# Performance work log

Hardware: AMD Instinct MI355X
Metric: run time of the kernel (lower is better)

## Reference

```python
import jax, jax.numpy as jnp
import numpy as np


def setup_inputs() -> dict:
    key = jax.random.key(0)
    k0, k1, k2, k3, k4 = jax.random.split(key, 5)
    B, d_inner, L, d_state = 64, 384, 197, 16
    x = jax.random.normal(k0, (B, d_inner, L), dtype=jnp.float32)
    # deltaA = exp(delta*A) lies in (0,1); uniform keeps the recurrence stable
    deltaA = jax.random.uniform(k1, (B, d_inner, L, d_state), dtype=jnp.float32)
    deltaB = jax.random.normal(k2, (B, d_inner, L, d_state), dtype=jnp.float32)
    C = jax.random.normal(k3, (B, d_state, L), dtype=jnp.float32)
    D = jax.random.normal(k4, (d_inner,), dtype=jnp.float32)
    return {"x": x, "deltaA": deltaA, "deltaB": deltaB, "C": C, "D": D}


def reference(x, deltaA, deltaB, C, D):
    """Selective scan: h_t = deltaB_t*x_t + deltaA_t*h_{t-1}; y_t = h_t @ C_t.
    x:(B,d,L) deltaA/deltaB:(B,d,L,n) C:(B,n,L) D:(d,)
    """
    deltaB_x = deltaB * x[..., None]              # (B,d,L,n)
    dA_t = jnp.moveaxis(deltaA, 2, 0)             # (L,B,d,n)
    dBx_t = jnp.moveaxis(deltaB_x, 2, 0)          # (L,B,d,n)
    C_t = jnp.moveaxis(C, 2, 0)                   # (L,B,n)

    def step(h, inputs):
        a, bx, c = inputs
        h = bx + a * h                            # (B,d,n)
        y = jnp.einsum("bdn,bn->bd", h, c)        # (B,d)
        return h, y

    h0 = jnp.zeros(dA_t.shape[1:], dtype=x.dtype)
    _, ys = jax.lax.scan(step, h0, (dA_t, dBx_t, C_t))  # ys: (L,B,d)
    y = jnp.moveaxis(ys, 0, 2)                    # (B,d,L)
    return y + x * D[:, None]
```

## Files before the change

kernel.cpp:

```cpp
#include <hip/hip_runtime.h>


#define B_   64
#define DIN  384
#define L_   197
#define N_   16
#define GRP_PER_BLOCK 32

__global__ __launch_bounds__(128)
void ssm_scan4(const float* __restrict__ x,
               const float* __restrict__ dA,
               const float* __restrict__ dB,
               const float* __restrict__ C,
               const float* __restrict__ D,
               float* __restrict__ y)
{
    __shared__ float Cs[L_ * N_];

    const int tid = threadIdx.x;
    const int b   = blockIdx.y;

    const float* Cg = C + (size_t)b * (N_ * L_);
    for (int i = tid; i < N_ * L_; i += 128) {
        const int n = i / L_;
        const int t = i - n * L_;
        Cs[t * N_ + n] = Cg[i];
    }
    __syncthreads();

    const int grp = tid >> 2;
    const int n4  = tid & 3;
    const int d   = blockIdx.x * GRP_PER_BLOCK + grp;

    const size_t bd = (size_t)b * DIN + d;
    const float4* pA = (const float4*)dA + bd * (size_t)(L_ * 4) + n4;
    const float4* pB = (const float4*)dB + bd * (size_t)(L_ * 4) + n4;
    const float*  px = x + bd * L_;
    float*        py = y + bd * L_;
    const float   Dd = D[d];

    float h0 = 0.f, h1 = 0.f, h2 = 0.f, h3 = 0.f;
    int t = 0;

    for (; t + 4 <= L_; t += 4) {
        const float4 a0 = pA[(t+0)*4], a1 = pA[(t+1)*4];
        const float4 a2 = pA[(t+2)*4], a3 = pA[(t+3)*4];
        const float4 g0 = pB[(t+0)*4], g1 = pB[(t+1)*4];
        const float4 g2 = pB[(t+2)*4], g3 = pB[(t+3)*4];
        const float  x0 = px[t+0], x1 = px[t+1], x2 = px[t+2], x3 = px[t+3];
        const float4 c0 = *(const float4*)(Cs + (t+0)*N_ + n4*4);
        const float4 c1 = *(const float4*)(Cs + (t+1)*N_ + n4*4);
        const float4 c2 = *(const float4*)(Cs + (t+2)*N_ + n4*4);
        const float4 c3 = *(const float4*)(Cs + (t+3)*N_ + n4*4);

        h0 = fmaf(a0.x, h0, g0.x * x0);
        h1 = fmaf(a0.y, h1, g0.y * x0);
        h2 = fmaf(a0.z, h2, g0.z * x0);
        h3 = fmaf(a0.w, h3, g0.w * x0);
        float p0 = fmaf(h0, c0.x, fmaf(h1, c0.y, fmaf(h2, c0.z, h3 * c0.w)));

        h0 = fmaf(a1.x, h0, g1.x * x1);
        h1 = fmaf(a1.y, h1, g1.y * x1);
        h2 = fmaf(a1.z, h2, g1.z * x1);
        h3 = fmaf(a1.w, h3, g1.w * x1);
        float p1 = fmaf(h0, c1.x, fmaf(h1, c1.y, fmaf(h2, c1.z, h3 * c1.w)));

        h0 = fmaf(a2.x, h0, g2.x * x2);
        h1 = fmaf(a2.y, h1, g2.y * x2);
        h2 = fmaf(a2.z, h2, g2.z * x2);
        h3 = fmaf(a2.w, h3, g2.w * x2);
        float p2 = fmaf(h0, c2.x, fmaf(h1, c2.y, fmaf(h2, c2.z, h3 * c2.w)));

        h0 = fmaf(a3.x, h0, g3.x * x3);
        h1 = fmaf(a3.y, h1, g3.y * x3);
        h2 = fmaf(a3.z, h2, g3.z * x3);
        h3 = fmaf(a3.w, h3, g3.w * x3);
        float p3 = fmaf(h0, c3.x, fmaf(h1, c3.y, fmaf(h2, c3.z, h3 * c3.w)));

        p0 += __shfl_xor(p0, 1);  p0 += __shfl_xor(p0, 2);
        p1 += __shfl_xor(p1, 1);  p1 += __shfl_xor(p1, 2);
        p2 += __shfl_xor(p2, 1);  p2 += __shfl_xor(p2, 2);
        p3 += __shfl_xor(p3, 1);  p3 += __shfl_xor(p3, 2);

        const float y0 = fmaf(x0, Dd, p0);
        const float y1 = fmaf(x1, Dd, p1);
        const float y2 = fmaf(x2, Dd, p2);
        const float y3 = fmaf(x3, Dd, p3);
        float yv = (n4 == 0) ? y0 : (n4 == 1) ? y1 : (n4 == 2) ? y2 : y3;
        py[t + n4] = yv;
    }

    for (; t < L_; ++t) {
        const float4 a = pA[t*4];
        const float4 g = pB[t*4];
        const float  xv = px[t];
        const float4 c = *(const float4*)(Cs + t*N_ + n4*4);
        h0 = fmaf(a.x, h0, g.x * xv);
        h1 = fmaf(a.y, h1, g.y * xv);
        h2 = fmaf(a.z, h2, g.z * xv);
        h3 = fmaf(a.w, h3, g.w * xv);
        float p = fmaf(h0, c.x, fmaf(h1, c.y, fmaf(h2, c.z, h3 * c.w)));
        p += __shfl_xor(p, 1);
        p += __shfl_xor(p, 2);
        if (n4 == 0) py[t] = fmaf(xv, Dd, p);
    }
}

extern "C" void kernel_launch(void* const* d_in, const int* in_sizes, int n_in,
                              void* d_out, int out_size, void* d_ws, size_t ws_size,
                              hipStream_t stream) {
    const float* x  = (const float*)d_in[0];
    const float* dA = (const float*)d_in[1];
    const float* dB = (const float*)d_in[2];
    const float* C  = (const float*)d_in[3];
    const float* D  = (const float*)d_in[4];
    float* y = (float*)d_out;

    dim3 grid(DIN / GRP_PER_BLOCK, B_);
    dim3 block(128);
    ssm_scan4<<<grid, block, 0, stream>>>(x, dA, dB, C, D, y);
}
```

Baseline: 156.9 us.

## Software-pipeline scan loads with triple register buffering

Restructures the time loop into a triple-buffered software pipeline: loads for chunk k+2 are issued before the recurrence for chunk k, so global memory latency overlaps the serial FMA chain. Launch bounds are set to one block minimum, which lets the compiler use more registers to hold the three buffers. The larger register footprint may reduce occupancy and hence the number of waves available to hide latency.

Result: faster. 150.8 us (-3.9%).

```diff
diff --git a/kernel.cpp b/kernel.cpp
--- a/kernel.cpp
+++ b/kernel.cpp
@@ -7,15 +7,15 @@
 #define N_   16
 #define GRP_PER_BLOCK 32
 
-__global__ __launch_bounds__(128)
-void ssm_scan4(const float* __restrict__ x,
-               const float* __restrict__ dA,
-               const float* __restrict__ dB,
-               const float* __restrict__ C,
-               const float* __restrict__ D,
-               float* __restrict__ y)
+__global__ __launch_bounds__(128, 1)
+void ssm_scan_pipe(const float* __restrict__ x,
+                   const float* __restrict__ dA,
+                   const float* __restrict__ dB,
+                   const float* __restrict__ C,
+                   const float* __restrict__ D,
+                   float* __restrict__ y)
 {
-    __shared__ float Cs[L_ * N_];
+    __shared__ __align__(16) float Cs[L_ * N_];
 
     const int tid = threadIdx.x;
     const int b   = blockIdx.y;
@@ -38,63 +38,62 @@
     const float*  px = x + bd * L_;
     float*        py = y + bd * L_;
     const float   Dd = D[d];
+    const float*  CsL = Cs + n4 * 4;
 
     float h0 = 0.f, h1 = 0.f, h2 = 0.f, h3 = 0.f;
-    int t = 0;
 
-    for (; t + 4 <= L_; t += 4) {
-        const float4 a0 = pA[(t+0)*4], a1 = pA[(t+1)*4];
-        const float4 a2 = pA[(t+2)*4], a3 = pA[(t+3)*4];
-        const float4 g0 = pB[(t+0)*4], g1 = pB[(t+1)*4];
-        const float4 g2 = pB[(t+2)*4], g3 = pB[(t+3)*4];
-        const float  x0 = px[t+0], x1 = px[t+1], x2 = px[t+2], x3 = px[t+3];
-        const float4 c0 = *(const float4*)(Cs + (t+0)*N_ + n4*4);
-        const float4 c1 = *(const float4*)(Cs + (t+1)*N_ + n4*4);
-        const float4 c2 = *(const float4*)(Cs + (t+2)*N_ + n4*4);
-        const float4 c3 = *(const float4*)(Cs + (t+3)*N_ + n4*4);
+#define DECLBUF(Bu) float4 Bu##a0,Bu##a1,Bu##a2,Bu##a3, Bu##g0,Bu##g1,Bu##g2,Bu##g3, \
+                            Bu##c0,Bu##c1,Bu##c2,Bu##c3; \
+                    float  Bu##x0,Bu##x1,Bu##x2,Bu##x3;
+    DECLBUF(B0) DECLBUF(B1) DECLBUF(B2)
 
-        h0 = fmaf(a0.x, h0, g0.x * x0);
-        h1 = fmaf(a0.y, h1, g0.y * x0);
-        h2 = fmaf(a0.z, h2, g0.z * x0);
-        h3 = fmaf(a0.w, h3, g0.w * x0);
-        float p0 = fmaf(h0, c0.x, fmaf(h1, c0.y, fmaf(h2, c0.z, h3 * c0.w)));
+#define LOADB(Bu, k) do { const int tt=(k)*4; \
+    Bu##a0=pA[(tt+0)*4]; Bu##a1=pA[(tt+1)*4]; Bu##a2=pA[(tt+2)*4]; Bu##a3=pA[(tt+3)*4]; \
+    Bu##g0=pB[(tt+0)*4]; Bu##g1=pB[(tt+1)*4]; Bu##g2=pB[(tt+2)*4]; Bu##g3=pB[(tt+3)*4]; \
+    Bu##x0=px[tt+0]; Bu##x1=px[tt+1]; Bu##x2=px[tt+2]; Bu##x3=px[tt+3]; \
+    Bu##c0=*(const float4*)(CsL+(tt+0)*N_); Bu##c1=*(const float4*)(CsL+(tt+1)*N_); \
+    Bu##c2=*(const float4*)(CsL+(tt+2)*N_); Bu##c3=*(const float4*)(CsL+(tt+3)*N_); \
+  } while(0)
 
-        h0 = fmaf(a1.x, h0, g1.x * x1);
-        h1 = fmaf(a1.y, h1, g1.y * x1);
-        h2 = fmaf(a1.z, h2, g1.z * x1);
-        h3 = fmaf(a1.w, h3, g1.w * x1);
-        float p1 = fmaf(h0, c1.x, fmaf(h1, c1.y, fmaf(h2, c1.z, h3 * c1.w)));
+#define COMPB(Bu, k) do { const int tt=(k)*4; \
+    h0=fmaf(Bu##a0.x,h0,Bu##g0.x*Bu##x0); h1=fmaf(Bu##a0.y,h1,Bu##g0.y*Bu##x0); \
+    h2=fmaf(Bu##a0.z,h2,Bu##g0.z*Bu##x0); h3=fmaf(Bu##a0.w,h3,Bu##g0.w*Bu##x0); \
+    float p0=fmaf(h0,Bu##c0.x,fmaf(h1,Bu##c0.y,fmaf(h2,Bu##c0.z,h3*Bu##c0.w))); \
+    h0=fmaf(Bu##a1.x,h0,Bu##g1.x*Bu##x1); h1=fmaf(Bu##a1.y,h1,Bu##g1.y*Bu##x1); \
+    h2=fmaf(Bu##a1.z,h2,Bu##g1.z*Bu##x1); h3=fmaf(Bu##a1.w,h3,Bu##g1.w*Bu##x1); \
+    float p1=fmaf(h0,Bu##c1.x,fmaf(h1,Bu##c1.y,fmaf(h2,Bu##c1.z,h3*Bu##c1.w))); \
+    h0=fmaf(Bu##a2.x,h0,Bu##g2.x*Bu##x2); h1=fmaf(Bu##a2.y,h1,Bu##g2.y*Bu##x2); \
+    h2=fmaf(Bu##a2.z,h2,Bu##g2.z*Bu##x2); h3=fmaf(Bu##a2.w,h3,Bu##g2.w*Bu##x2); \
+    float p2=fmaf(h0,Bu##c2.x,fmaf(h1,Bu##c2.y,fmaf(h2,Bu##c2.z,h3*Bu##c2.w))); \
+    h0=fmaf(Bu##a3.x,h0,Bu##g3.x*Bu##x3); h1=fmaf(Bu##a3.y,h1,Bu##g3.y*Bu##x3); \
+    h2=fmaf(Bu##a3.z,h2,Bu##g3.z*Bu##x3); h3=fmaf(Bu##a3.w,h3,Bu##g3.w*Bu##x3); \
+    float p3=fmaf(h0,Bu##c3.x,fmaf(h1,Bu##c3.y,fmaf(h2,Bu##c3.z,h3*Bu##c3.w))); \
+    p0+=__shfl_xor(p0,1); p1+=__shfl_xor(p1,1); p2+=__shfl_xor(p2,1); p3+=__shfl_xor(p3,1); \
+    p0+=__shfl_xor(p0,2); p1+=__shfl_xor(p1,2); p2+=__shfl_xor(p2,2); p3+=__shfl_xor(p3,2); \
+    const float yv = (n4==0)?fmaf(Bu##x0,Dd,p0):(n4==1)?fmaf(Bu##x1,Dd,p1): \
+                     (n4==2)?fmaf(Bu##x2,Dd,p2):fmaf(Bu##x3,Dd,p3); \
+    py[tt+n4]=yv; \
+  } while(0)
 
-        h0 = fmaf(a2.x, h0, g2.x * x2);
-        h1 = fmaf(a2.y, h1, g2.y * x2);
-        h2 = fmaf(a2.z, h2, g2.z * x2);
-        h3 = fmaf(a2.w, h3, g2.w * x2);
-        float p2 = fmaf(h0, c2.x, fmaf(h1, c2.y, fmaf(h2, c2.z, h3 * c2.w)));
+    LOADB(B0, 0);
+    LOADB(B1, 1);
 
-        h0 = fmaf(a3.x, h0, g3.x * x3);
-        h1 = fmaf(a3.y, h1, g3.y * x3);
-        h2 = fmaf(a3.z, h2, g3.z * x3);
-        h3 = fmaf(a3.w, h3, g3.w * x3);
-        float p3 = fmaf(h0, c3.x, fmaf(h1, c3.y, fmaf(h2, c3.z, h3 * c3.w)));
+    for (int k = 0; k <= 42; k += 3) {
+        LOADB(B2, k+2);  COMPB(B0, k);
+        LOADB(B0, k+3);  COMPB(B1, k+1);
+        LOADB(B1, k+4);  COMPB(B2, k+2);
+    }
+    LOADB(B2, 47);  COMPB(B0, 45);
+    LOADB(B0, 48);  COMPB(B1, 46);
+    COMPB(B2, 47);
+    COMPB(B0, 48);
 
-        p0 += __shfl_xor(p0, 1);  p0 += __shfl_xor(p0, 2);
-        p1 += __shfl_xor(p1, 1);  p1 += __shfl_xor(p1, 2);
-        p2 += __shfl_xor(p2, 1);  p2 += __shfl_xor(p2, 2);
-        p3 += __shfl_xor(p3, 1);  p3 += __shfl_xor(p3, 2);
-
-        const float y0 = fmaf(x0, Dd, p0);
-        const float y1 = fmaf(x1, Dd, p1);
-        const float y2 = fmaf(x2, Dd, p2);
-        const float y3 = fmaf(x3, Dd, p3);
-        float yv = (n4 == 0) ? y0 : (n4 == 1) ? y1 : (n4 == 2) ? y2 : y3;
-        py[t + n4] = yv;
-    }
-
-    for (; t < L_; ++t) {
+    {
+        const int t = 196;
         const float4 a = pA[t*4];
         const float4 g = pB[t*4];
         const float  xv = px[t];
-        const float4 c = *(const float4*)(Cs + t*N_ + n4*4);
+        const float4 c = *(const float4*)(CsL + t*N_);
         h0 = fmaf(a.x, h0, g.x * xv);
         h1 = fmaf(a.y, h1, g.y * xv);
         h2 = fmaf(a.z, h2, g.z * xv);
@@ -118,5 +117,5 @@
 
     dim3 grid(DIN / GRP_PER_BLOCK, B_);
     dim3 block(128);
-    ssm_scan4<<<grid, block, 0, stream>>>(x, dA, dB, C, D, y);
+    ssm_scan_pipe<<<grid, block, 0, stream>>>(x, dA, dB, C, D, y);
 }
```
